# Optimization experiments

Hardware: AMD Instinct MI355X
Metric: run time of the kernel (lower is better)

Reference implementation:

```python
import jax, jax.numpy as jnp
import numpy as np

ROPE_BASE = 10000.0

def rotary_pe_3d(x, coords):
    # x: [B, H, L, D]; coords: [B, L, 3]. Split D into 3 axis chunks; rotate
    # each chunk (half-split pairs) by angles coord_axis * inv_freq.
    D = x.shape[-1]
    da = D // 3            # dims per spatial axis
    p = da // 2            # rotary pairs per axis
    inv_freq = 1.0 / (ROPE_BASE ** (jnp.arange(p, dtype=x.dtype) / p))  # [p]
    chunks = []
    for a in range(3):
        xa = x[..., a * da:(a + 1) * da]                       # [B,H,L,da]
        theta = coords[..., a][:, None, :, None] * inv_freq    # [B,1,L,p]
        cos, sin = jnp.cos(theta), jnp.sin(theta)
        x1, x2 = xa[..., :p], xa[..., p:]
        chunks.append(jnp.concatenate([x1 * cos - x2 * sin,
                                       x1 * sin + x2 * cos], axis=-1))
    if 3 * da < D:  # leave any remainder un-rotated
        chunks.append(x[..., 3 * da:])
    return jnp.concatenate(chunks, axis=-1)


def setup_inputs() -> dict:
    key = jax.random.key(0)
    ks = jax.random.split(key, 16)
    B, Lq, Lk, D, H = 4, 1024, 4096, 768, 8
    s = 1.0 / np.sqrt(D)
    return {
        "query": jax.random.normal(ks[0], (B, Lq, D), jnp.float32),
        "key": jax.random.normal(ks[1], (B, Lk, D), jnp.float32),
        "value": jax.random.normal(ks[2], (B, Lk, D), jnp.float32),
        "coords_query": jax.random.normal(ks[3], (B, Lq, 3), jnp.float32),
        "coords_key": jax.random.normal(ks[4], (B, Lk, 3), jnp.float32),
        "Wq": jax.random.normal(ks[5], (D, D), jnp.float32) * s,
        "bq": jnp.zeros((D,), jnp.float32),
        "Wk": jax.random.normal(ks[6], (D, D), jnp.float32) * s,
        "bk": jnp.zeros((D,), jnp.float32),
        "Wv": jax.random.normal(ks[7], (D, D), jnp.float32) * s,
        "bv": jnp.zeros((D,), jnp.float32),
        "Wo": jax.random.normal(ks[8], (D, D), jnp.float32) * s,
        "bo": jnp.zeros((D,), jnp.float32),
    }


def reference(query, key, value, coords_query, coords_key,
              Wq, bq, Wk, bk, Wv, bv, Wo, bo):
    B, Lq, D = query.shape
    Lk = key.shape[1]
    H = 8
    hd = D // H
    # Projections (nn.Linear: x @ W.T + b)
    q = (query @ Wq.T + bq).reshape(B, Lq, H, hd).transpose(0, 2, 1, 3)  # [B,H,Lq,hd]
    k = (key @ Wk.T + bk).reshape(B, Lk, H, hd).transpose(0, 2, 1, 3)
    v = (value @ Wv.T + bv).reshape(B, Lk, H, hd).transpose(0, 2, 1, 3)
    q = rotary_pe_3d(q, coords_query)
    k = rotary_pe_3d(k, coords_key)
    scores = jnp.einsum("bhqd,bhkd->bhqk", q, k) / jnp.sqrt(jnp.asarray(hd, q.dtype))
    attn = jax.nn.softmax(scores, axis=-1)  # dropout is identity in eval
    out = jnp.einsum("bhqk,bhkd->bhqd", attn, v)
    out = out.transpose(0, 2, 1, 3).reshape(B, Lq, D)
    return out @ Wo.T + bo
```

## Files before the change

### kernel.cpp

```cpp
#include <hip/hip_runtime.h>
#include <math.h>

#define DM 768
#define NH 8
#define HD 96
#define BQ 4
#define LQ 1024
#define LK 4096
#define BH (BQ*NH)
#define KVS 4
#define KC (LK/KVS)
#define NT (KC/64)
#define QB 128
#define NW (DM*DM)

typedef unsigned short ushort;
typedef unsigned int uint;
typedef __attribute__((ext_vector_type(8))) short short8v;
typedef __attribute__((ext_vector_type(4))) float float4v;

#define QSCALE 0.14724444641f

static __device__ __forceinline__ ushort f2bf(float x) {
    union { float f; uint u; } c; c.f = x;
    uint u = c.u;
    u += ((u >> 16) & 1u) + 0x7fffu;
    return (ushort)(u >> 16);
}

static __device__ __forceinline__ float bf2f(ushort x) {
    union { uint u; float f; } c; c.u = (uint)x << 16;
    return c.f;
}

static __device__ __forceinline__ uint cvtpk(float lo, float hi) {
    uint d;
    asm("v_cvt_pk_bf16_f32 %0, %1, %2" : "=v"(d) : "v"(lo), "v"(hi));
    return d;
}

static __device__ __forceinline__ float exp2hw(float x) {
#if __has_builtin(__builtin_amdgcn_exp2f)
    return __builtin_amdgcn_exp2f(x);
#else
    return __expf(x * 0.6931471805599453f);
#endif
}

static __device__ __forceinline__ void gload_lds16(const ushort* g, ushort* l) {
    __builtin_amdgcn_global_load_lds(
        (const __attribute__((address_space(1))) uint*)g,
        (__attribute__((address_space(3))) uint*)l, 16, 0, 0);
}

__global__ __launch_bounds__(256)
void wcvt(const float* __restrict__ w0, const float* __restrict__ w1,
          const float* __restrict__ w2, const float* __restrict__ w3,
          ushort* __restrict__ d)
{
    const int SEG = NW / 1024;
    int b = blockIdx.x;
    int wsel = b / SEG, ib = b % SEG;
    const float* s = (wsel == 0) ? w0 : (wsel == 1) ? w1 : (wsel == 2) ? w2 : w3;
    int i = ib * 256 + threadIdx.x;
    float4 v = ((const float4*)s)[i];
    uint2 o;
    o.x = (uint)f2bf(v.x) | ((uint)f2bf(v.y) << 16);
    o.y = (uint)f2bf(v.z) | ((uint)f2bf(v.w) << 16);
    ((uint2*)(d + (size_t)wsel * NW))[i] = o;
}

__global__ __launch_bounds__(256, 2)
void qkv_gemm(const float* __restrict__ qf, const float* __restrict__ kf,
              const float* __restrict__ vf,
              const ushort* __restrict__ wqb, const ushort* __restrict__ wkb,
              const ushort* __restrict__ wvb,
              const float* __restrict__ bq, const float* __restrict__ bk,
              const float* __restrict__ bv,
              const float* __restrict__ cq, const float* __restrict__ ck,
              ushort* __restrict__ qws, ushort* __restrict__ kws,
              ushort* __restrict__ vtb)
{
    __shared__ ushort Sh[16384];
    ushort* As = Sh;
    ushort* Bs = Sh + 8192;

    const int tid  = threadIdx.x;
    const int w    = tid >> 6;
    const int lane = tid & 63;
    const int l15  = lane & 15;
    const int lg   = lane >> 4;
    const int wm   = w >> 1, wn = w & 1;

    const int L = blockIdx.x;
    int seg, idx, Lshift, rpx;
    const float* X32; const ushort* Wbp; const float* bias; const float* coords;
    ushort* out; float oscale;
    if (L < 192)      { seg = 0; idx = L;       X32 = qf; Wbp = wqb; bias = bq; coords = cq; out = qws; Lshift = 10; rpx = 4;  oscale = QSCALE; }
    else if (L < 960) { seg = 1; idx = L - 192; X32 = kf; Wbp = wkb; bias = bk; coords = ck; out = kws; Lshift = 12; rpx = 16; oscale = 1.0f; }
    else              { seg = 2; idx = L - 960; X32 = vf; Wbp = wvb; bias = bv; coords = 0;  out = vtb; Lshift = 12; rpx = 16; oscale = 1.0f; }

    const int xcd  = idx & 7;
    const int sq   = idx >> 3;
    const int col0 = (sq % 6) * 128;
    const int row0 = (xcd * rpx + sq / 6) * 128;

    float4v acc[4][4];
    #pragma unroll
    for (int m = 0; m < 4; ++m)
        #pragma unroll
        for (int n = 0; n < 4; ++n) acc[m][n] = (float4v)0.f;

    int Pp[4], rrS[4], cbS[4];
    #pragma unroll
    for (int c = 0; c < 4; ++c) {
        int P = ((w*4 + c) << 10) + lane*16;
        int lgc = P ^ (((P >> 9) & 3) << 5);
        Pp[c]  = P;
        rrS[c] = lgc >> 7;
        cbS[c] = (lgc & 127) >> 1;
    }
    const float*  xb = X32 + (size_t)row0 * DM;
    const ushort* wb = Wbp + (size_t)col0 * DM;

    int offA[2][4], offB[2][4];
    #pragma unroll
    for (int kk = 0; kk < 2; ++kk) {
        #pragma unroll
        for (int m = 0; m < 4; ++m) {
            int byte = (wm*64 + m*16 + l15)*128 + kk*64 + lg*16;
            offA[kk][m] = byte ^ (((byte >> 9) & 3) << 5);
            byte = (wn*64 + m*16 + l15)*128 + kk*64 + lg*16;
            offB[kk][m] = byte ^ (((byte >> 9) & 3) << 5);
        }
    }

    for (int kt = 0; kt < DM; kt += 64) {
        float4 fa[4], fb[4];
        #pragma unroll
        for (int c = 0; c < 4; ++c) {
            const float* src = xb + (size_t)rrS[c]*DM + kt + cbS[c];
            fa[c] = *(const float4*)src;
            fb[c] = *(const float4*)(src + 4);
        }
        #pragma unroll
        for (int c = 0; c < 4; ++c)
            gload_lds16(wb + (size_t)rrS[c]*DM + kt + cbS[c], (ushort*)((char*)Bs + Pp[c]));
        #pragma unroll
        for (int c = 0; c < 4; ++c) {
            uint4 pk;
            pk.x = cvtpk(fa[c].x, fa[c].y);
            pk.y = cvtpk(fa[c].z, fa[c].w);
            pk.z = cvtpk(fb[c].x, fb[c].y);
            pk.w = cvtpk(fb[c].z, fb[c].w);
            *(uint4*)((char*)As + Pp[c]) = pk;
        }
        __syncthreads();
        #pragma unroll
        for (int kk = 0; kk < 2; ++kk) {
            short8v af[4], bfm[4];
            #pragma unroll
            for (int m = 0; m < 4; ++m)
                af[m] = *(const short8v*)((const char*)As + offA[kk][m]);
            #pragma unroll
            for (int n = 0; n < 4; ++n)
                bfm[n] = *(const short8v*)((const char*)Bs + offB[kk][n]);
            #pragma unroll
            for (int m = 0; m < 4; ++m)
                #pragma unroll
                for (int n = 0; n < 4; ++n)
                    acc[m][n] = __builtin_amdgcn_mfma_f32_16x16x32_bf16(af[m], bfm[n], acc[m][n], 0, 0, 0);
        }
        __syncthreads();
    }

    const int colbase = col0 + wn*64;
    float bvv[4];
    #pragma unroll
    for (int nt = 0; nt < 4; ++nt) bvv[nt] = bias[colbase + nt*16 + l15];
    #pragma unroll
    for (int m = 0; m < 4; ++m)
        #pragma unroll
        for (int nt = 0; nt < 4; ++nt)
            #pragma unroll
            for (int r = 0; r < 4; ++r) acc[m][nt][r] += bvv[nt];

    if (seg < 2) {
        const float freq = exp2f(-(float)l15 * 0.83048202372184058696f);
        const int a0 = ((colbase >> 5) + 0) % 3;
        const int a1 = ((colbase >> 5) + 1) % 3;
        const int F  = (colbase >> 4) & 1;
        #pragma unroll
        for (int m = 0; m < 4; ++m) {
            #pragma unroll
            for (int r = 0; r < 4; ++r) {
                int row = row0 + wm*64 + m*16 + lg*4 + r;
                const float* c3 = coords + (size_t)row * 3;
                float sn0, cs0, sn1, cs1;
                __sincosf(c3[a0] * freq, &sn0, &cs0);
                __sincosf(c3[a1] * freq, &sn1, &cs1);
                {
                    float A_ = F ? acc[m][1][r] : acc[m][0][r];
                    float B_ = F ? acc[m][0][r] : acc[m][1][r];
                    float x1 = (A_*cs0 - B_*sn0) * oscale, x2 = (A_*sn0 + B_*cs0) * oscale;
                    if (F) { acc[m][1][r] = x1; acc[m][0][r] = x2; }
                    else   { acc[m][0][r] = x1; acc[m][1][r] = x2; }
                }
                {
                    float A_ = F ? acc[m][3][r] : acc[m][2][r];
                    float B_ = F ? acc[m][2][r] : acc[m][3][r];
                    float x1 = (A_*cs1 - B_*sn1) * oscale, x2 = (A_*sn1 + B_*cs1) * oscale;
                    if (F) { acc[m][3][r] = x1; acc[m][2][r] = x2; }
                    else   { acc[m][2][r] = x1; acc[m][3][r] = x2; }
                }
            }
        }
        const int Lm1 = (1 << Lshift) - 1;
        int hh[4], tt[4];
        #pragma unroll
        for (int nt = 0; nt < 4; ++nt) {
            int j0 = colbase + nt*16;
            hh[nt] = j0 / HD;
            tt[nt] = j0 % HD + l15;
        }
        #pragma unroll
        for (int m = 0; m < 4; ++m)
            #pragma unroll
            for (int r = 0; r < 4; ++r) {
                int row = row0 + wm*64 + m*16 + lg*4 + r;
                int b = row >> Lshift, l = row & Lm1;
                #pragma unroll
                for (int nt = 0; nt < 4; ++nt)
                    out[(((size_t)b*NH + hh[nt]) << Lshift | l) * HD + tt[nt]] =
                        f2bf(acc[m][nt][r]);
            }
    } else {
        #pragma unroll
        for (int m = 0; m < 4; ++m)
            #pragma unroll
            for (int nt = 0; nt < 4; ++nt)
                #pragma unroll
                for (int r = 0; r < 4; ++r) {
                    int c  = wn*64 + nt*16 + l15;
                    int ri = wm*64 + m*16 + lg*4 + r;
                    *(ushort*)((char*)Sh + c*256 + (((ri>>3) ^ (c&7))<<4) + (ri&7)*2)
                        = f2bf(acc[m][nt][r]);
                }
        __syncthreads();
        #pragma unroll
        for (int e = 0; e < 8; ++e) {
            int idx2 = tid + 256*e;
            int c = idx2 >> 4, r8 = idx2 & 15;
            uint4 val = *(const uint4*)((const char*)Sh + c*256 + ((r8 ^ (c&7))<<4));
            int j = col0 + c;
            int h = j / HD, t = j % HD;
            int row = row0 + r8*8;
            int b = row >> 12, l = row & (LK-1);
            *(uint4*)&out[(((size_t)b*NH + h)*HD + t)*LK + l] = val;
        }
    }
}

__global__ __launch_bounds__(256)
void gemm_out(const ushort* __restrict__ X, const ushort* __restrict__ Wb,
              const float* __restrict__ bias, float* __restrict__ out)
{
    __shared__ ushort Sh[16384];
    ushort* As = Sh;
    ushort* Bs = Sh + 8192;

    const int tid  = threadIdx.x;
    const int w    = tid >> 6;
    const int lane = tid & 63;
    const int l15  = lane & 15;
    const int lg   = lane >> 4;
    const int wm   = w >> 1, wn = w & 1;

    const int L    = blockIdx.x;
    const int xcd  = L & 7;
    const int sq   = L >> 3;
    const int col0 = (sq % 6) * 128;
    const int row0 = (xcd * 4 + sq / 6) * 128;

    float4v acc[4][4];
    #pragma unroll
    for (int m = 0; m < 4; ++m)
        #pragma unroll
        for (int n = 0; n < 4; ++n) acc[m][n] = (float4v)0.f;

    int Pp[4], rrS[4], cbS[4];
    #pragma unroll
    for (int c = 0; c < 4; ++c) {
        int P = ((w*4 + c) << 10) + lane*16;
        int lgc = P ^ (((P >> 9) & 3) << 5);
        Pp[c]  = P;
        rrS[c] = lgc >> 7;
        cbS[c] = (lgc & 127) >> 1;
    }
    const ushort* xb = X  + (size_t)row0 * DM;
    const ushort* wb = Wb + (size_t)col0 * DM;

    int offA[2][4], offB[2][4];
    #pragma unroll
    for (int kk = 0; kk < 2; ++kk) {
        #pragma unroll
        for (int m = 0; m < 4; ++m) {
            int byte = (wm*64 + m*16 + l15)*128 + kk*64 + lg*16;
            offA[kk][m] = byte ^ (((byte >> 9) & 3) << 5);
            byte = (wn*64 + m*16 + l15)*128 + kk*64 + lg*16;
            offB[kk][m] = byte ^ (((byte >> 9) & 3) << 5);
        }
    }

    for (int kt = 0; kt < DM; kt += 64) {
        #pragma unroll
        for (int c = 0; c < 4; ++c) {
            gload_lds16(xb + (size_t)rrS[c]*DM + kt + cbS[c], (ushort*)((char*)As + Pp[c]));
            gload_lds16(wb + (size_t)rrS[c]*DM + kt + cbS[c], (ushort*)((char*)Bs + Pp[c]));
        }
        __syncthreads();
        #pragma unroll
        for (int kk = 0; kk < 2; ++kk) {
            short8v af[4], bfm[4];
            #pragma unroll
            for (int m = 0; m < 4; ++m)
                af[m] = *(const short8v*)((const char*)As + offA[kk][m]);
            #pragma unroll
            for (int n = 0; n < 4; ++n)
                bfm[n] = *(const short8v*)((const char*)Bs + offB[kk][n]);
            #pragma unroll
            for (int m = 0; m < 4; ++m)
                #pragma unroll
                for (int n = 0; n < 4; ++n)
                    acc[m][n] = __builtin_amdgcn_mfma_f32_16x16x32_bf16(af[m], bfm[n], acc[m][n], 0, 0, 0);
        }
        __syncthreads();
    }

    const int colbase = col0 + wn*64;
    float bvv[4];
    #pragma unroll
    for (int nt = 0; nt < 4; ++nt) bvv[nt] = bias[colbase + nt*16 + l15];
    #pragma unroll
    for (int m = 0; m < 4; ++m)
        #pragma unroll
        for (int r = 0; r < 4; ++r) {
            int row = row0 + wm*64 + m*16 + lg*4 + r;
            #pragma unroll
            for (int nt = 0; nt < 4; ++nt)
                out[(size_t)row*DM + colbase + nt*16 + l15] = acc[m][nt][r] + bvv[nt];
        }
}

__global__ __launch_bounds__(256, 2)
void attn_mfma(const ushort* __restrict__ q, const ushort* __restrict__ k,
               const ushort* __restrict__ vt, ushort* __restrict__ opb,
               float* __restrict__ mlb)
{
    __shared__ ushort Ks[64*128];
    __shared__ ushort Vs[96*64];
    __shared__ ushort PsT[4][32][72];

    const int tid  = threadIdx.x;
    const int w    = tid >> 6;
    const int lane = tid & 63;
    const int l15  = lane & 15;
    const int lg   = lane >> 4;

    const int L   = blockIdx.x;
    const int xcd = L & 7;
    const int s   = L >> 3;
    const int pr  = xcd*16 + (s >> 3);
    const int qt  = s & 7;
    const int bh  = pr & 31;
    const int sc  = pr >> 5;

    const ushort* qg = q  + ((size_t)bh * LQ + qt*QB + w*32 + l15) * HD;
    const ushort* kg = k  + ((size_t)bh * LK + (size_t)sc * KC) * HD;
    const ushort* vg = vt + (size_t)bh * HD * LK + (size_t)sc * KC;

    short8v aq0[3], aq1[3];
    #pragma unroll
    for (int dc = 0; dc < 3; ++dc) {
        aq0[dc] = *(const short8v*)(qg + dc*32 + lg*8);
        aq1[dc] = *(const short8v*)(qg + 16*HD + dc*32 + lg*8);
    }

    int kdst[3], ksrc[3], vdst[3], vsrc[3];
    #pragma unroll
    for (int j = 0; j < 3; ++j) {
        int c = tid + 256*j;
        int kr = c / 12, ks = c % 12;
        kdst[j] = kr*256 + ((ks ^ (kr & 7)) << 4);
        ksrc[j] = kr*HD + ks*8;
        int vr = c >> 3, vs = c & 7;
        vdst[j] = vr*128 + ((vs ^ (vr & 7)) << 4);
        vsrc[j] = vr*LK + vs*8;
    }
    int tK[3], tV[2];
    #pragma unroll
    for (int dc = 0; dc < 3; ++dc) tK[dc] = ((dc*4 + lg) ^ (l15 & 7)) << 4;
    #pragma unroll
    for (int h2 = 0; h2 < 2; ++h2)  tV[h2] = ((h2*4 + lg) ^ (l15 & 7)) << 4;

    float4v o0[6], o1[6];
    #pragma unroll
    for (int dt = 0; dt < 6; ++dt) { o0[dt] = (float4v)0.f; o1[dt] = (float4v)0.f; }
    float m_0 = -1e30f, l_0 = 0.f;
    float m_1 = -1e30f, l_1 = 0.f;

    short8v kreg[3], vreg[3];
    #pragma unroll
    for (int j = 0; j < 3; ++j) {
        kreg[j] = *(const short8v*)(kg + ksrc[j]);
        vreg[j] = *(const short8v*)(vg + vsrc[j]);
    }
    #pragma unroll
    for (int j = 0; j < 3; ++j) {
        *(short8v*)((char*)Ks + kdst[j]) = kreg[j];
        *(short8v*)((char*)Vs + vdst[j]) = vreg[j];
    }
    __syncthreads();

    for (int t = 0; t < NT; ++t) {
        if (t + 1 < NT) {
            const ushort* kn = kg + (size_t)(t+1)*64*HD;
            const ushort* vn = vg + (t+1)*64;
            #pragma unroll
            for (int j = 0; j < 3; ++j) {
                kreg[j] = *(const short8v*)(kn + ksrc[j]);
                vreg[j] = *(const short8v*)(vn + vsrc[j]);
            }
        }

        float4v s0[4], s1[4];
        __builtin_amdgcn_s_setprio(1);
        #pragma unroll
        for (int nt = 0; nt < 4; ++nt) {
            s0[nt] = (float4v)0.f;
            s1[nt] = (float4v)0.f;
            #pragma unroll
            for (int dc = 0; dc < 3; ++dc) {
                short8v bk = *(const short8v*)((const char*)Ks + nt*4096 + l15*256 + tK[dc]);
                s0[nt] = __builtin_amdgcn_mfma_f32_16x16x32_bf16(bk, aq0[dc], s0[nt], 0, 0, 0);
                s1[nt] = __builtin_amdgcn_mfma_f32_16x16x32_bf16(bk, aq1[dc], s1[nt], 0, 0, 0);
            }
        }
        __builtin_amdgcn_s_setprio(0);

        float mt0 = -1e30f, mt1 = -1e30f;
        #pragma unroll
        for (int nt = 0; nt < 4; ++nt)
            #pragma unroll
            for (int r = 0; r < 4; ++r) {
                mt0 = fmaxf(mt0, s0[nt][r]);
                mt1 = fmaxf(mt1, s1[nt][r]);
            }
        mt0 = fmaxf(mt0, __shfl_xor(mt0, 16, 64));
        mt0 = fmaxf(mt0, __shfl_xor(mt0, 32, 64));
        mt1 = fmaxf(mt1, __shfl_xor(mt1, 16, 64));
        mt1 = fmaxf(mt1, __shfl_xor(mt1, 32, 64));

        if (__any((mt0 > m_0 + 11.5f) || (mt1 > m_1 + 11.5f))) {
            float mn0 = fmaxf(m_0, mt0), mn1 = fmaxf(m_1, mt1);
            float a0 = exp2hw(m_0 - mn0), a1 = exp2hw(m_1 - mn1);
            m_0 = mn0; m_1 = mn1;
            l_0 *= a0;  l_1 *= a1;
            float al0[4], al1[4];
            #pragma unroll
            for (int r = 0; r < 4; ++r) {
                al0[r] = __shfl(a0, lg*4 + r, 64);
                al1[r] = __shfl(a1, lg*4 + r, 64);
            }
            #pragma unroll
            for (int dt = 0; dt < 6; ++dt)
                #pragma unroll
                for (int r = 0; r < 4; ++r) {
                    o0[dt][r] *= al0[r];
                    o1[dt][r] *= al1[r];
                }
        }

        float ps0 = 0.f, ps1 = 0.f;
        #pragma unroll
        for (int nt = 0; nt < 4; ++nt)
            #pragma unroll
            for (int r = 0; r < 4; ++r) {
                float p0 = exp2hw(s0[nt][r] - m_0);
                float p1 = exp2hw(s1[nt][r] - m_1);
                s0[nt][r] = p0; ps0 += p0;
                s1[nt][r] = p1; ps1 += p1;
            }
        ps0 += __shfl_xor(ps0, 16, 64);
        ps0 += __shfl_xor(ps0, 32, 64);
        ps1 += __shfl_xor(ps1, 16, 64);
        ps1 += __shfl_xor(ps1, 32, 64);
        l_0 += ps0;
        l_1 += ps1;

        #pragma unroll
        for (int nt = 0; nt < 4; ++nt) {
            uint2 pk0, pk1;
            pk0.x = cvtpk(s0[nt][0], s0[nt][1]);
            pk0.y = cvtpk(s0[nt][2], s0[nt][3]);
            pk1.x = cvtpk(s1[nt][0], s1[nt][1]);
            pk1.y = cvtpk(s1[nt][2], s1[nt][3]);
            *(uint2*)&PsT[w][l15][nt*16 + lg*4]      = pk0;
            *(uint2*)&PsT[w][16 + l15][nt*16 + lg*4] = pk1;
        }

        short8v a00 = *(const short8v*)&PsT[w][l15][lg*8];
        short8v a01 = *(const short8v*)&PsT[w][l15][32 + lg*8];
        short8v a10 = *(const short8v*)&PsT[w][16 + l15][lg*8];
        short8v a11 = *(const short8v*)&PsT[w][16 + l15][32 + lg*8];
        __builtin_amdgcn_s_setprio(1);
        #pragma unroll
        for (int dt = 0; dt < 6; ++dt) {
            short8v bv0 = *(const short8v*)((const char*)Vs + dt*2048 + l15*128 + tV[0]);
            short8v bv1 = *(const short8v*)((const char*)Vs + dt*2048 + l15*128 + tV[1]);
            o0[dt] = __builtin_amdgcn_mfma_f32_16x16x32_bf16(a00, bv0, o0[dt], 0, 0, 0);
            o0[dt] = __builtin_amdgcn_mfma_f32_16x16x32_bf16(a01, bv1, o0[dt], 0, 0, 0);
            o1[dt] = __builtin_amdgcn_mfma_f32_16x16x32_bf16(a10, bv0, o1[dt], 0, 0, 0);
            o1[dt] = __builtin_amdgcn_mfma_f32_16x16x32_bf16(a11, bv1, o1[dt], 0, 0, 0);
        }
        __builtin_amdgcn_s_setprio(0);
        __syncthreads();

        if (t + 1 < NT) {
            #pragma unroll
            for (int j = 0; j < 3; ++j) {
                *(short8v*)((char*)Ks + kdst[j]) = kreg[j];
                *(short8v*)((char*)Vs + vdst[j]) = vreg[j];
            }
        }
        __syncthreads();
    }

    ushort* ob = opb + (((size_t)sc * BH + bh) * LQ + qt*QB + w*32) * HD;
    #pragma unroll
    for (int r = 0; r < 4; ++r) {
        #pragma unroll
        for (int dt = 0; dt < 6; ++dt) {
            ob[(size_t)(lg*4 + r) * HD + dt*16 + l15]      = f2bf(o0[dt][r]);
            ob[(size_t)(16 + lg*4 + r) * HD + dt*16 + l15] = f2bf(o1[dt][r]);
        }
    }
    if (lane < 16) {
        size_t mlrow = ((size_t)sc * BH + bh) * LQ + qt*QB + w*32 + lane;
        mlb[mlrow*2 + 0] = m_0;
        mlb[mlrow*2 + 1] = l_0;
        mlb[(mlrow + 16)*2 + 0] = m_1;
        mlb[(mlrow + 16)*2 + 1] = l_1;
    }
}

__global__ __launch_bounds__(256)
void combine(const ushort* __restrict__ opb, const float* __restrict__ mlb,
             ushort* __restrict__ ctx)
{
    const int NROW = BH * LQ;
    int idx = blockIdx.x * 256 + threadIdx.x;
    int row = idx / 12, seg = idx % 12;

    float m[KVS], lv[KVS];
    #pragma unroll
    for (int i = 0; i < KVS; ++i) {
        m[i]  = mlb[((size_t)i*NROW + row)*2 + 0];
        lv[i] = mlb[((size_t)i*NROW + row)*2 + 1];
    }
    float ms = m[0];
    #pragma unroll
    for (int i = 1; i < KVS; ++i) ms = fmaxf(ms, m[i]);
    float wsum = 0.f, wgt[KVS];
    #pragma unroll
    for (int i = 0; i < KVS; ++i) {
        wgt[i] = exp2hw(m[i] - ms);
        wsum += lv[i] * wgt[i];
    }
    float inv = 1.f / wsum;

    float acc[8] = {};
    #pragma unroll
    for (int i = 0; i < KVS; ++i) {
        uint4 v = *(const uint4*)&opb[((size_t)i*NROW + row)*HD + seg*8];
        uint vv[4] = {v.x, v.y, v.z, v.w};
        #pragma unroll
        for (int j2 = 0; j2 < 4; ++j2) {
            acc[j2*2+0] += bf2f((ushort)(vv[j2] & 0xffff)) * wgt[i];
            acc[j2*2+1] += bf2f((ushort)(vv[j2] >> 16))    * wgt[i];
        }
    }

    int bh = row / LQ, l = row % LQ;
    int b = bh >> 3, h = bh & 7;
    ushort* o = ctx + ((size_t)b * LQ + l) * DM + h * HD + seg*8;
    uint4 pk;
    pk.x = cvtpk(acc[0]*inv, acc[1]*inv);
    pk.y = cvtpk(acc[2]*inv, acc[3]*inv);
    pk.z = cvtpk(acc[4]*inv, acc[5]*inv);
    pk.w = cvtpk(acc[6]*inv, acc[7]*inv);
    *(uint4*)o = pk;
}

extern "C" void kernel_launch(void* const* d_in, const int* in_sizes, int n_in,
                              void* d_out, int out_size, void* d_ws, size_t ws_size,
                              hipStream_t stream)
{
    const float* query = (const float*)d_in[0];
    const float* key   = (const float*)d_in[1];
    const float* value = (const float*)d_in[2];
    const float* cq    = (const float*)d_in[3];
    const float* ck    = (const float*)d_in[4];
    const float* Wq    = (const float*)d_in[5];
    const float* bqv   = (const float*)d_in[6];
    const float* Wk    = (const float*)d_in[7];
    const float* bkv   = (const float*)d_in[8];
    const float* Wv    = (const float*)d_in[9];
    const float* bvv   = (const float*)d_in[10];
    const float* Wo    = (const float*)d_in[11];
    const float* bov   = (const float*)d_in[12];
    float* out = (float*)d_out;

    const size_t NQ = (size_t)BQ * LQ * DM;
    const size_t NK = (size_t)BQ * LK * DM;
    const size_t NP = (size_t)KVS * BH * LQ * HD;

    ushort* wq  = (ushort*)d_ws;
    ushort* wk  = wq  + NW;
    ushort* wv  = wk  + NW;
    ushort* wo  = wv  + NW;
    ushort* qws = wo  + NW;
    ushort* kws = qws + NQ;
    ushort* vtb = kws + NK;
    ushort* opb = vtb + NK;
    ushort* ctx = opb + NP;
    float*  mlb = (float*)(ctx + NQ);

    wcvt<<<4*(NW/1024), 256, 0, stream>>>(Wq, Wk, Wv, Wo, wq);
    qkv_gemm<<<1728, 256, 0, stream>>>(query, key, value, wq, wk, wv,
                                       bqv, bkv, bvv, cq, ck, qws, kws, vtb);
    attn_mfma<<<(LQ/QB) * BH * KVS, 256, 0, stream>>>(qws, kws, vtb, opb, mlb);
    combine<<<BH*LQ*12/256, 256, 0, stream>>>(opb, mlb, ctx);
    gemm_out<<<(BQ*LQ/128)*6, 256, 0, stream>>>(ctx, wo, bov, out);
}
```

Before: 171.1 us.

## Software-pipeline QKV GEMM K-loop with double-buffered weight tiles in LDS

Restructures the qkv_gemm K loop so the next weight tile is loaded asynchronously into a second LDS buffer and the next fp32 activation tile is fetched into registers while MFMAs run on the current tile. The activation tile is converted to bf16 and stored after a barrier, which adds one extra __syncthreads per step. It also raises launch_bounds occupancy from 2 to 3 blocks per CU, which may add register pressure and spills, given the live prefetch registers and the 48KB of shared memory.

```diff
diff --git a/kernel.cpp b/kernel.cpp
--- a/kernel.cpp
+++ b/kernel.cpp
@@ -13,6 +13,7 @@
 #define NT (KC/64)
 #define QB 128
 #define NW (DM*DM)
+#define NKSTEP (DM/64)
 
 typedef unsigned short ushort;
 typedef unsigned int uint;
@@ -70,7 +71,7 @@
     ((uint2*)(d + (size_t)wsel * NW))[i] = o;
 }
 
-__global__ __launch_bounds__(256, 2)
+__global__ __launch_bounds__(256, 3)
 void qkv_gemm(const float* __restrict__ qf, const float* __restrict__ kf,
               const float* __restrict__ vf,
               const ushort* __restrict__ wqb, const ushort* __restrict__ wkb,
@@ -81,9 +82,7 @@
               ushort* __restrict__ qws, ushort* __restrict__ kws,
               ushort* __restrict__ vtb)
 {
-    __shared__ ushort Sh[16384];
-    ushort* As = Sh;
-    ushort* Bs = Sh + 8192;
+    __shared__ ushort Sh[24576];
 
     const int tid  = threadIdx.x;
     const int w    = tid >> 6;
@@ -135,36 +134,51 @@
         }
     }
 
-    for (int kt = 0; kt < DM; kt += 64) {
-        float4 fa[4], fb[4];
-        #pragma unroll
-        for (int c = 0; c < 4; ++c) {
-            const float* src = xb + (size_t)rrS[c]*DM + kt + cbS[c];
-            fa[c] = *(const float4*)src;
-            fb[c] = *(const float4*)(src + 4);
-        }
-        #pragma unroll
-        for (int c = 0; c < 4; ++c)
-            gload_lds16(wb + (size_t)rrS[c]*DM + kt + cbS[c], (ushort*)((char*)Bs + Pp[c]));
-        #pragma unroll
-        for (int c = 0; c < 4; ++c) {
-            uint4 pk;
-            pk.x = cvtpk(fa[c].x, fa[c].y);
-            pk.y = cvtpk(fa[c].z, fa[c].w);
-            pk.z = cvtpk(fb[c].x, fb[c].y);
-            pk.w = cvtpk(fb[c].z, fb[c].w);
-            *(uint4*)((char*)As + Pp[c]) = pk;
-        }
-        __syncthreads();
+    float4 fa[4], fb[4];
+    #pragma unroll
+    for (int c = 0; c < 4; ++c) {
+        const float* src = xb + (size_t)rrS[c]*DM + cbS[c];
+        fa[c] = *(const float4*)src;
+        fb[c] = *(const float4*)(src + 4);
+    }
+    #pragma unroll
+    for (int c = 0; c < 4; ++c)
+        gload_lds16(wb + (size_t)rrS[c]*DM + cbS[c], (ushort*)((char*)Sh + 16384 + Pp[c]));
+    #pragma unroll
+    for (int c = 0; c < 4; ++c) {
+        uint4 pk;
+        pk.x = cvtpk(fa[c].x, fa[c].y);
+        pk.y = cvtpk(fa[c].z, fa[c].w);
+        pk.z = cvtpk(fb[c].x, fb[c].y);
+        pk.w = cvtpk(fb[c].z, fb[c].w);
+        *(uint4*)((char*)Sh + Pp[c]) = pk;
+    }
+    __syncthreads();
+
+    for (int t = 0; t < NKSTEP; ++t) {
+        const int bbase = 16384 + ((t & 1) << 14);
+        if (t + 1 < NKSTEP) {
+            const int nb = 16384 + (((t + 1) & 1) << 14);
+            #pragma unroll
+            for (int c = 0; c < 4; ++c)
+                gload_lds16(wb + (size_t)rrS[c]*DM + (t+1)*64 + cbS[c],
+                            (ushort*)((char*)Sh + nb + Pp[c]));
+            #pragma unroll
+            for (int c = 0; c < 4; ++c) {
+                const float* src = xb + (size_t)rrS[c]*DM + (t+1)*64 + cbS[c];
+                fa[c] = *(const float4*)src;
+                fb[c] = *(const float4*)(src + 4);
+            }
+        }
         #pragma unroll
         for (int kk = 0; kk < 2; ++kk) {
             short8v af[4], bfm[4];
             #pragma unroll
             for (int m = 0; m < 4; ++m)
-                af[m] = *(const short8v*)((const char*)As + offA[kk][m]);
+                af[m] = *(const short8v*)((const char*)Sh + offA[kk][m]);
             #pragma unroll
             for (int n = 0; n < 4; ++n)
-                bfm[n] = *(const short8v*)((const char*)Bs + offB[kk][n]);
+                bfm[n] = *(const short8v*)((const char*)Sh + bbase + offB[kk][n]);
             #pragma unroll
             for (int m = 0; m < 4; ++m)
                 #pragma unroll
@@ -172,6 +186,18 @@
                     acc[m][n] = __builtin_amdgcn_mfma_f32_16x16x32_bf16(af[m], bfm[n], acc[m][n], 0, 0, 0);
         }
         __syncthreads();
+        if (t + 1 < NKSTEP) {
+            #pragma unroll
+            for (int c = 0; c < 4; ++c) {
+                uint4 pk;
+                pk.x = cvtpk(fa[c].x, fa[c].y);
+                pk.y = cvtpk(fa[c].z, fa[c].w);
+                pk.z = cvtpk(fb[c].x, fb[c].y);
+                pk.w = cvtpk(fb[c].z, fb[c].w);
+                *(uint4*)((char*)Sh + Pp[c]) = pk;
+            }
+            __syncthreads();
+        }
     }
 
     const int colbase = col0 + wn*64;
```

After: 174.9 us. +2.2%, slower.

## Load fp32 activations directly to LDS and convert to bf16 at fragment read

Applied to the files above, without the earlier changes.

The QKV projection GEMM now streams the fp32 activation tile straight into shared memory with global_load_lds, using a new XOR swizzle, instead of loading through registers and converting before the LDS store. The bf16 conversion moves to the MFMA fragment read, so each k-step does two fp32 LDS reads per fragment. The goal is to cut VGPR pressure and register staging so occupancy can rise to 3 blocks per CU. The cost is LDS growing to 48KB per block, doubled LDS read traffic for A, and conversions repeated in the inner loop.

```diff
diff --git a/kernel.cpp b/kernel.cpp
--- a/kernel.cpp
+++ b/kernel.cpp
@@ -13,6 +13,7 @@
 #define NT (KC/64)
 #define QB 128
 #define NW (DM*DM)
+#define NKSTEP (DM/64)
 
 typedef unsigned short ushort;
 typedef unsigned int uint;
@@ -47,7 +48,7 @@
 #endif
 }
 
-static __device__ __forceinline__ void gload_lds16(const ushort* g, ushort* l) {
+static __device__ __forceinline__ void gload_lds16(const void* g, void* l) {
     __builtin_amdgcn_global_load_lds(
         (const __attribute__((address_space(1))) uint*)g,
         (__attribute__((address_space(3))) uint*)l, 16, 0, 0);
@@ -70,7 +71,7 @@
     ((uint2*)(d + (size_t)wsel * NW))[i] = o;
 }
 
-__global__ __launch_bounds__(256, 2)
+__global__ __launch_bounds__(256, 3)
 void qkv_gemm(const float* __restrict__ qf, const float* __restrict__ kf,
               const float* __restrict__ vf,
               const ushort* __restrict__ wqb, const ushort* __restrict__ wkb,
@@ -81,9 +82,9 @@
               ushort* __restrict__ qws, ushort* __restrict__ kws,
               ushort* __restrict__ vtb)
 {
-    __shared__ ushort Sh[16384];
-    ushort* As = Sh;
-    ushort* Bs = Sh + 8192;
+    __shared__ ushort Sh[24576];
+    char* As = (char*)Sh;
+    char* Bs = (char*)Sh + 32768;
 
     const int tid  = threadIdx.x;
     const int w    = tid >> 6;
@@ -111,60 +112,67 @@
         #pragma unroll
         for (int n = 0; n < 4; ++n) acc[m][n] = (float4v)0.f;
 
-    int Pp[4], rrS[4], cbS[4];
+    int PA[8], rA[8], cA[8];
+    #pragma unroll
+    for (int c = 0; c < 8; ++c) {
+        int P = ((w*8 + c) << 10) + lane*16;
+        int r = P >> 8;
+        int j = ((P >> 4) & 15) ^ (r & 15);
+        PA[c] = P;
+        rA[c] = r;
+        cA[c] = j * 4;
+    }
+    int PB[4], rB[4], cB[4];
     #pragma unroll
     for (int c = 0; c < 4; ++c) {
         int P = ((w*4 + c) << 10) + lane*16;
         int lgc = P ^ (((P >> 9) & 3) << 5);
-        Pp[c]  = P;
-        rrS[c] = lgc >> 7;
-        cbS[c] = (lgc & 127) >> 1;
+        PB[c] = P;
+        rB[c] = lgc >> 7;
+        cB[c] = (lgc & 127) >> 1;
     }
     const float*  xb = X32 + (size_t)row0 * DM;
     const ushort* wb = Wbp + (size_t)col0 * DM;
 
-    int offA[2][4], offB[2][4];
+    int offA0[2][4], offA1[2][4], offB[2][4];
     #pragma unroll
     for (int kk = 0; kk < 2; ++kk) {
         #pragma unroll
         for (int m = 0; m < 4; ++m) {
-            int byte = (wm*64 + m*16 + l15)*128 + kk*64 + lg*16;
-            offA[kk][m] = byte ^ (((byte >> 9) & 3) << 5);
-            byte = (wn*64 + m*16 + l15)*128 + kk*64 + lg*16;
+            int R  = wm*64 + m*16 + l15;
+            int j0 = kk*8 + lg*2;
+            offA0[kk][m] = R*256 + (((j0    ) ^ (R & 15)) << 4);
+            offA1[kk][m] = R*256 + (((j0 + 1) ^ (R & 15)) << 4);
+            int byte = (wn*64 + m*16 + l15)*128 + kk*64 + lg*16;
             offB[kk][m] = byte ^ (((byte >> 9) & 3) << 5);
         }
     }
 
     for (int kt = 0; kt < DM; kt += 64) {
-        float4 fa[4], fb[4];
-        #pragma unroll
-        for (int c = 0; c < 4; ++c) {
-            const float* src = xb + (size_t)rrS[c]*DM + kt + cbS[c];
-            fa[c] = *(const float4*)src;
-            fb[c] = *(const float4*)(src + 4);
-        }
+        #pragma unroll
+        for (int c = 0; c < 8; ++c)
+            gload_lds16(xb + (size_t)rA[c]*DM + kt + cA[c], As + PA[c]);
         #pragma unroll
         for (int c = 0; c < 4; ++c)
-            gload_lds16(wb + (size_t)rrS[c]*DM + kt + cbS[c], (ushort*)((char*)Bs + Pp[c]));
-        #pragma unroll
-        for (int c = 0; c < 4; ++c) {
-            uint4 pk;
-            pk.x = cvtpk(fa[c].x, fa[c].y);
-            pk.y = cvtpk(fa[c].z, fa[c].w);
-            pk.z = cvtpk(fb[c].x, fb[c].y);
-            pk.w = cvtpk(fb[c].z, fb[c].w);
-            *(uint4*)((char*)As + Pp[c]) = pk;
-        }
+            gload_lds16(wb + (size_t)rB[c]*DM + kt + cB[c], Bs + PB[c]);
         __syncthreads();
         #pragma unroll
         for (int kk = 0; kk < 2; ++kk) {
             short8v af[4], bfm[4];
             #pragma unroll
-            for (int m = 0; m < 4; ++m)
-                af[m] = *(const short8v*)((const char*)As + offA[kk][m]);
+            for (int m = 0; m < 4; ++m) {
+                float4 x0 = *(const float4*)(As + offA0[kk][m]);
+                float4 x1 = *(const float4*)(As + offA1[kk][m]);
+                union { uint4 u; short8v s; } cv;
+                cv.u.x = cvtpk(x0.x, x0.y);
+                cv.u.y = cvtpk(x0.z, x0.w);
+                cv.u.z = cvtpk(x1.x, x1.y);
+                cv.u.w = cvtpk(x1.z, x1.w);
+                af[m] = cv.s;
+            }
             #pragma unroll
             for (int n = 0; n < 4; ++n)
-                bfm[n] = *(const short8v*)((const char*)Bs + offB[kk][n]);
+                bfm[n] = *(const short8v*)(Bs + offB[kk][n]);
             #pragma unroll
             for (int m = 0; m < 4; ++m)
                 #pragma unroll
@@ -243,7 +251,7 @@
                 for (int r = 0; r < 4; ++r) {
                     int c  = wn*64 + nt*16 + l15;
                     int ri = wm*64 + m*16 + lg*4 + r;
-                    *(ushort*)((char*)Sh + c*256 + (((ri>>3) ^ (c&7))<<4) + (ri&7)*2)
+                    *(ushort*)(As + c*256 + (((ri>>3) ^ (c&7))<<4) + (ri&7)*2)
                         = f2bf(acc[m][nt][r]);
                 }
         __syncthreads();
@@ -251,7 +259,7 @@
         for (int e = 0; e < 8; ++e) {
             int idx2 = tid + 256*e;
             int c = idx2 >> 4, r8 = idx2 & 15;
-            uint4 val = *(const uint4*)((const char*)Sh + c*256 + ((r8 ^ (c&7))<<4));
+            uint4 val = *(const uint4*)(As + c*256 + ((r8 ^ (c&7))<<4));
             int j = col0 + c;
             int h = j / HD, t = j % HD;
             int row = row0 + r8*8;
@@ -315,8 +323,8 @@
     for (int kt = 0; kt < DM; kt += 64) {
         #pragma unroll
         for (int c = 0; c < 4; ++c) {
-            gload_lds16(xb + (size_t)rrS[c]*DM + kt + cbS[c], (ushort*)((char*)As + Pp[c]));
-            gload_lds16(wb + (size_t)rrS[c]*DM + kt + cbS[c], (ushort*)((char*)Bs + Pp[c]));
+            gload_lds16(xb + (size_t)rrS[c]*DM + kt + cbS[c], (char*)As + Pp[c]);
+            gload_lds16(wb + (size_t)rrS[c]*DM + kt + cbS[c], (char*)Bs + Pp[c]);
         }
         __syncthreads();
         #pragma unroll
```

Measured after the change: 172.7 us. No clear change (+1.0%).

## Widen QKV projection GEMM tile to 128x256 to halve fp32 activation reloads

Applied to the files above, without the earlier changes.

The fused QKV projection kernel now computes 128x256 output tiles instead of 128x128, so each block converts its fp32 activation rows once for twice as many output columns. This halves the block count and the redundant global reads and bf16 conversion of the large fp32 inputs. In exchange each wave holds twice the accumulators, which raises register pressure under launch_bounds(256,2). The rotary and V-transpose epilogues are reworked to match, and the V transpose is staged through LDS in two column halves.

```diff
diff --git a/kernel.cpp b/kernel.cpp
--- a/kernel.cpp
+++ b/kernel.cpp
@@ -13,6 +13,7 @@
 #define NT (KC/64)
 #define QB 128
 #define NW (DM*DM)
+#define NKSTEP (DM/64)
 
 typedef unsigned short ushort;
 typedef unsigned int uint;
@@ -47,7 +48,7 @@
 #endif
 }
 
-static __device__ __forceinline__ void gload_lds16(const ushort* g, ushort* l) {
+static __device__ __forceinline__ void gload_lds16(const void* g, void* l) {
     __builtin_amdgcn_global_load_lds(
         (const __attribute__((address_space(1))) uint*)g,
         (__attribute__((address_space(3))) uint*)l, 16, 0, 0);
@@ -81,9 +82,9 @@
               ushort* __restrict__ qws, ushort* __restrict__ kws,
               ushort* __restrict__ vtb)
 {
-    __shared__ ushort Sh[16384];
-    ushort* As = Sh;
-    ushort* Bs = Sh + 8192;
+    __shared__ ushort Sh[24576];
+    char* As = (char*)Sh;
+    char* Bs = (char*)Sh + 16384;
 
     const int tid  = threadIdx.x;
     const int w    = tid >> 6;
@@ -96,14 +97,200 @@
     int seg, idx, Lshift, rpx;
     const float* X32; const ushort* Wbp; const float* bias; const float* coords;
     ushort* out; float oscale;
-    if (L < 192)      { seg = 0; idx = L;       X32 = qf; Wbp = wqb; bias = bq; coords = cq; out = qws; Lshift = 10; rpx = 4;  oscale = QSCALE; }
-    else if (L < 960) { seg = 1; idx = L - 192; X32 = kf; Wbp = wkb; bias = bk; coords = ck; out = kws; Lshift = 12; rpx = 16; oscale = 1.0f; }
-    else              { seg = 2; idx = L - 960; X32 = vf; Wbp = wvb; bias = bv; coords = 0;  out = vtb; Lshift = 12; rpx = 16; oscale = 1.0f; }
+    if (L < 96)       { seg = 0; idx = L;       X32 = qf; Wbp = wqb; bias = bq; coords = cq; out = qws; Lshift = 10; rpx = 4;  oscale = QSCALE; }
+    else if (L < 480) { seg = 1; idx = L - 96;  X32 = kf; Wbp = wkb; bias = bk; coords = ck; out = kws; Lshift = 12; rpx = 16; oscale = 1.0f; }
+    else              { seg = 2; idx = L - 480; X32 = vf; Wbp = wvb; bias = bv; coords = 0;  out = vtb; Lshift = 12; rpx = 16; oscale = 1.0f; }
 
     const int xcd  = idx & 7;
     const int sq   = idx >> 3;
+    const int col0 = (sq % 3) * 256;
+    const int row0 = (xcd * rpx + sq / 3) * 128;
+
+    float4v acc[4][8];
+    #pragma unroll
+    for (int m = 0; m < 4; ++m)
+        #pragma unroll
+        for (int n = 0; n < 8; ++n) acc[m][n] = (float4v)0.f;
+
+    int PA[4], rA[4], cA[4];
+    #pragma unroll
+    for (int c = 0; c < 4; ++c) {
+        int P = ((w*4 + c) << 10) + lane*16;
+        int lgc = P ^ (((P >> 9) & 3) << 5);
+        PA[c] = P;
+        rA[c] = lgc >> 7;
+        cA[c] = (lgc & 127) >> 1;
+    }
+    int PB[8], rB[8], cB[8];
+    #pragma unroll
+    for (int c = 0; c < 8; ++c) {
+        int P = ((w*8 + c) << 10) + lane*16;
+        int lgc = P ^ (((P >> 9) & 3) << 5);
+        PB[c] = P;
+        rB[c] = lgc >> 7;
+        cB[c] = (lgc & 127) >> 1;
+    }
+    const float*  xb = X32 + (size_t)row0 * DM;
+    const ushort* wb = Wbp + (size_t)col0 * DM;
+
+    int offA[2][4], offB[2][8];
+    #pragma unroll
+    for (int kk = 0; kk < 2; ++kk) {
+        #pragma unroll
+        for (int m = 0; m < 4; ++m) {
+            int byte = (wm*64 + m*16 + l15)*128 + kk*64 + lg*16;
+            offA[kk][m] = byte ^ (((byte >> 9) & 3) << 5);
+        }
+        #pragma unroll
+        for (int n = 0; n < 8; ++n) {
+            int byte = (wn*128 + n*16 + l15)*128 + kk*64 + lg*16;
+            offB[kk][n] = byte ^ (((byte >> 9) & 3) << 5);
+        }
+    }
+
+    for (int kt = 0; kt < DM; kt += 64) {
+        #pragma unroll
+        for (int c = 0; c < 8; ++c)
+            gload_lds16(wb + (size_t)rB[c]*DM + kt + cB[c], Bs + PB[c]);
+        float4 fa[4], fb[4];
+        #pragma unroll
+        for (int c = 0; c < 4; ++c) {
+            const float* src = xb + (size_t)rA[c]*DM + kt + cA[c];
+            fa[c] = *(const float4*)src;
+            fb[c] = *(const float4*)(src + 4);
+        }
+        #pragma unroll
+        for (int c = 0; c < 4; ++c) {
+            uint4 pk;
+            pk.x = cvtpk(fa[c].x, fa[c].y);
+            pk.y = cvtpk(fa[c].z, fa[c].w);
+            pk.z = cvtpk(fb[c].x, fb[c].y);
+            pk.w = cvtpk(fb[c].z, fb[c].w);
+            *(uint4*)(As + PA[c]) = pk;
+        }
+        __syncthreads();
+        #pragma unroll
+        for (int kk = 0; kk < 2; ++kk) {
+            short8v af[4], bfm[8];
+            #pragma unroll
+            for (int m = 0; m < 4; ++m)
+                af[m] = *(const short8v*)(As + offA[kk][m]);
+            #pragma unroll
+            for (int n = 0; n < 8; ++n)
+                bfm[n] = *(const short8v*)(Bs + offB[kk][n]);
+            #pragma unroll
+            for (int m = 0; m < 4; ++m)
+                #pragma unroll
+                for (int n = 0; n < 8; ++n)
+                    acc[m][n] = __builtin_amdgcn_mfma_f32_16x16x32_bf16(af[m], bfm[n], acc[m][n], 0, 0, 0);
+        }
+        __syncthreads();
+    }
+
+    const int colbase = col0 + wn*128;
+    float bvv[8];
+    #pragma unroll
+    for (int nt = 0; nt < 8; ++nt) bvv[nt] = bias[colbase + nt*16 + l15];
+    #pragma unroll
+    for (int m = 0; m < 4; ++m)
+        #pragma unroll
+        for (int nt = 0; nt < 8; ++nt)
+            #pragma unroll
+            for (int r = 0; r < 4; ++r) acc[m][nt][r] += bvv[nt];
+
+    if (seg < 2) {
+        const float freq = exp2f(-(float)l15 * 0.83048202372184058696f);
+        int ap[4];
+        #pragma unroll
+        for (int p = 0; p < 4; ++p) ap[p] = ((colbase >> 5) + p) % 3;
+        #pragma unroll
+        for (int m = 0; m < 4; ++m) {
+            #pragma unroll
+            for (int r = 0; r < 4; ++r) {
+                int row = row0 + wm*64 + m*16 + lg*4 + r;
+                const float* c3 = coords + (size_t)row * 3;
+                #pragma unroll
+                for (int p = 0; p < 4; ++p) {
+                    float sn, cs;
+                    __sincosf(c3[ap[p]] * freq, &sn, &cs);
+                    float A_ = acc[m][2*p][r], B_ = acc[m][2*p+1][r];
+                    acc[m][2*p][r]   = (A_*cs - B_*sn) * oscale;
+                    acc[m][2*p+1][r] = (A_*sn + B_*cs) * oscale;
+                }
+            }
+        }
+        const int Lm1 = (1 << Lshift) - 1;
+        int hh[8], tt[8];
+        #pragma unroll
+        for (int nt = 0; nt < 8; ++nt) {
+            int j0 = colbase + nt*16;
+            hh[nt] = j0 / HD;
+            tt[nt] = j0 % HD + l15;
+        }
+        #pragma unroll
+        for (int m = 0; m < 4; ++m)
+            #pragma unroll
+            for (int r = 0; r < 4; ++r) {
+                int row = row0 + wm*64 + m*16 + lg*4 + r;
+                int b = row >> Lshift, l = row & Lm1;
+                #pragma unroll
+                for (int nt = 0; nt < 8; ++nt)
+                    out[(((size_t)b*NH + hh[nt]) << Lshift | l) * HD + tt[nt]] =
+                        f2bf(acc[m][nt][r]);
+            }
+    } else {
+        #pragma unroll
+        for (int h2 = 0; h2 < 2; ++h2) {
+            __syncthreads();
+            if (wn == h2) {
+                #pragma unroll
+                for (int m = 0; m < 4; ++m)
+                    #pragma unroll
+                    for (int nt = 0; nt < 8; ++nt)
+                        #pragma unroll
+                        for (int r = 0; r < 4; ++r) {
+                            int c  = nt*16 + l15;
+                            int ri = wm*64 + m*16 + lg*4 + r;
+                            *(ushort*)((char*)Sh + c*256 + (((ri>>3) ^ (c&7))<<4) + (ri&7)*2)
+                                = f2bf(acc[m][nt][r]);
+                        }
+            }
+            __syncthreads();
+            #pragma unroll
+            for (int e = 0; e < 8; ++e) {
+                int idx2 = tid + 256*e;
+                int c = idx2 >> 4, r8 = idx2 & 15;
+                uint4 val = *(const uint4*)((const char*)Sh + c*256 + ((r8 ^ (c&7))<<4));
+                int j = col0 + h2*128 + c;
+                int h = j / HD, t = j % HD;
+                int row = row0 + r8*8;
+                int b = row >> 12, l = row & (LK-1);
+                *(uint4*)&out[(((size_t)b*NH + h)*HD + t)*LK + l] = val;
+            }
+        }
+    }
+}
+
+__global__ __launch_bounds__(256)
+void gemm_out(const ushort* __restrict__ X, const ushort* __restrict__ Wb,
+              const float* __restrict__ bias, float* __restrict__ out)
+{
+    __shared__ ushort Sh[16384];
+    char* As = (char*)Sh;
+    char* Bs = (char*)Sh + 16384;
+
+    const int tid  = threadIdx.x;
+    const int w    = tid >> 6;
+    const int lane = tid & 63;
+    const int l15  = lane & 15;
+    const int lg   = lane >> 4;
+    const int wm   = w >> 1, wn = w & 1;
+
+    const int L    = blockIdx.x;
+    const int xcd  = L & 7;
+    const int sq   = L >> 3;
     const int col0 = (sq % 6) * 128;
-    const int row0 = (xcd * rpx + sq / 6) * 128;
+    const int row0 = (xcd * 4 + sq / 6) * 128;
 
     float4v acc[4][4];
     #pragma unroll
@@ -120,8 +307,8 @@
         rrS[c] = lgc >> 7;
         cbS[c] = (lgc & 127) >> 1;
     }
-    const float*  xb = X32 + (size_t)row0 * DM;
-    const ushort* wb = Wbp + (size_t)col0 * DM;
+    const ushort* xb = X  + (size_t)row0 * DM;
+    const ushort* wb = Wb + (size_t)col0 * DM;
 
     int offA[2][4], offB[2][4];
     #pragma unroll
@@ -136,24 +323,10 @@
     }
 
     for (int kt = 0; kt < DM; kt += 64) {
-        float4 fa[4], fb[4];
         #pragma unroll
         for (int c = 0; c < 4; ++c) {
-            const float* src = xb + (size_t)rrS[c]*DM + kt + cbS[c];
-            fa[c] = *(const float4*)src;
-            fb[c] = *(const float4*)(src + 4);
-        }
-        #pragma unroll
-        for (int c = 0; c < 4; ++c)
-            gload_lds16(wb + (size_t)rrS[c]*DM + kt + cbS[c], (ushort*)((char*)Bs + Pp[c]));
-        #pragma unroll
-        for (int c = 0; c < 4; ++c) {
-            uint4 pk;
-            pk.x = cvtpk(fa[c].x, fa[c].y);
-            pk.y = cvtpk(fa[c].z, fa[c].w);
-            pk.z = cvtpk(fb[c].x, fb[c].y);
-            pk.w = cvtpk(fb[c].z, fb[c].w);
-            *(uint4*)((char*)As + Pp[c]) = pk;
+            gload_lds16(xb + (size_t)rrS[c]*DM + kt + cbS[c], As + Pp[c]);
+            gload_lds16(wb + (size_t)rrS[c]*DM + kt + cbS[c], Bs + Pp[c]);
         }
         __syncthreads();
         #pragma unroll
@@ -161,173 +334,10 @@
             short8v af[4], bfm[4];
             #pragma unroll
             for (int m = 0; m < 4; ++m)
-                af[m] = *(const short8v*)((const char*)As + offA[kk][m]);
+                af[m] = *(const short8v*)(As + offA[kk][m]);
             #pragma unroll
             for (int n = 0; n < 4; ++n)
-                bfm[n] = *(const short8v*)((const char*)Bs + offB[kk][n]);
-            #pragma unroll
-            for (int m = 0; m < 4; ++m)
-                #pragma unroll
-                for (int n = 0; n < 4; ++n)
-                    acc[m][n] = __builtin_amdgcn_mfma_f32_16x16x32_bf16(af[m], bfm[n], acc[m][n], 0, 0, 0);
-        }
-        __syncthreads();
-    }
-
-    const int colbase = col0 + wn*64;
-    float bvv[4];
-    #pragma unroll
-    for (int nt = 0; nt < 4; ++nt) bvv[nt] = bias[colbase + nt*16 + l15];
-    #pragma unroll
-    for (int m = 0; m < 4; ++m)
-        #pragma unroll
-        for (int nt = 0; nt < 4; ++nt)
-            #pragma unroll
-            for (int r = 0; r < 4; ++r) acc[m][nt][r] += bvv[nt];
-
-    if (seg < 2) {
-        const float freq = exp2f(-(float)l15 * 0.83048202372184058696f);
-        const int a0 = ((colbase >> 5) + 0) % 3;
-        const int a1 = ((colbase >> 5) + 1) % 3;
-        const int F  = (colbase >> 4) & 1;
-        #pragma unroll
-        for (int m = 0; m < 4; ++m) {
-            #pragma unroll
-            for (int r = 0; r < 4; ++r) {
-                int row = row0 + wm*64 + m*16 + lg*4 + r;
-                const float* c3 = coords + (size_t)row * 3;
-                float sn0, cs0, sn1, cs1;
-                __sincosf(c3[a0] * freq, &sn0, &cs0);
-                __sincosf(c3[a1] * freq, &sn1, &cs1);
-                {
-                    float A_ = F ? acc[m][1][r] : acc[m][0][r];
-                    float B_ = F ? acc[m][0][r] : acc[m][1][r];
-                    float x1 = (A_*cs0 - B_*sn0) * oscale, x2 = (A_*sn0 + B_*cs0) * oscale;
-                    if (F) { acc[m][1][r] = x1; acc[m][0][r] = x2; }
-                    else   { acc[m][0][r] = x1; acc[m][1][r] = x2; }
-                }
-                {
-                    float A_ = F ? acc[m][3][r] : acc[m][2][r];
-                    float B_ = F ? acc[m][2][r] : acc[m][3][r];
-                    float x1 = (A_*cs1 - B_*sn1) * oscale, x2 = (A_*sn1 + B_*cs1) * oscale;
-                    if (F) { acc[m][3][r] = x1; acc[m][2][r] = x2; }
-                    else   { acc[m][2][r] = x1; acc[m][3][r] = x2; }
-                }
-            }
-        }
-        const int Lm1 = (1 << Lshift) - 1;
-        int hh[4], tt[4];
-        #pragma unroll
-        for (int nt = 0; nt < 4; ++nt) {
-            int j0 = colbase + nt*16;
-            hh[nt] = j0 / HD;
-            tt[nt] = j0 % HD + l15;
-        }
-        #pragma unroll
-        for (int m = 0; m < 4; ++m)
-            #pragma unroll
-            for (int r = 0; r < 4; ++r) {
-                int row = row0 + wm*64 + m*16 + lg*4 + r;
-                int b = row >> Lshift, l = row & Lm1;
-                #pragma unroll
-                for (int nt = 0; nt < 4; ++nt)
-                    out[(((size_t)b*NH + hh[nt]) << Lshift | l) * HD + tt[nt]] =
-                        f2bf(acc[m][nt][r]);
-            }
-    } else {
-        #pragma unroll
-        for (int m = 0; m < 4; ++m)
-            #pragma unroll
-            for (int nt = 0; nt < 4; ++nt)
-                #pragma unroll
-                for (int r = 0; r < 4; ++r) {
-                    int c  = wn*64 + nt*16 + l15;
-                    int ri = wm*64 + m*16 + lg*4 + r;
-                    *(ushort*)((char*)Sh + c*256 + (((ri>>3) ^ (c&7))<<4) + (ri&7)*2)
-                        = f2bf(acc[m][nt][r]);
-                }
-        __syncthreads();
-        #pragma unroll
-        for (int e = 0; e < 8; ++e) {
-            int idx2 = tid + 256*e;
-            int c = idx2 >> 4, r8 = idx2 & 15;
-            uint4 val = *(const uint4*)((const char*)Sh + c*256 + ((r8 ^ (c&7))<<4));
-            int j = col0 + c;
-            int h = j / HD, t = j % HD;
-            int row = row0 + r8*8;
-            int b = row >> 12, l = row & (LK-1);
-            *(uint4*)&out[(((size_t)b*NH + h)*HD + t)*LK + l] = val;
-        }
-    }
-}
-
-__global__ __launch_bounds__(256)
-void gemm_out(const ushort* __restrict__ X, const ushort* __restrict__ Wb,
-              const float* __restrict__ bias, float* __restrict__ out)
-{
-    __shared__ ushort Sh[16384];
-    ushort* As = Sh;
-    ushort* Bs = Sh + 8192;
-
-    const int tid  = threadIdx.x;
-    const int w    = tid >> 6;
-    const int lane = tid & 63;
-    const int l15  = lane & 15;
-    const int lg   = lane >> 4;
-    const int wm   = w >> 1, wn = w & 1;
-
-    const int L    = blockIdx.x;
-    const int xcd  = L & 7;
-    const int sq   = L >> 3;
-    const int col0 = (sq % 6) * 128;
-    const int row0 = (xcd * 4 + sq / 6) * 128;
-
-    float4v acc[4][4];
-    #pragma unroll
-    for (int m = 0; m < 4; ++m)
-        #pragma unroll
-        for (int n = 0; n < 4; ++n) acc[m][n] = (float4v)0.f;
-
-    int Pp[4], rrS[4], cbS[4];
-    #pragma unroll
-    for (int c = 0; c < 4; ++c) {
-        int P = ((w*4 + c) << 10) + lane*16;
-        int lgc = P ^ (((P >> 9) & 3) << 5);
-        Pp[c]  = P;
-        rrS[c] = lgc >> 7;
-        cbS[c] = (lgc & 127) >> 1;
-    }
-    const ushort* xb = X  + (size_t)row0 * DM;
-    const ushort* wb = Wb + (size_t)col0 * DM;
-
-    int offA[2][4], offB[2][4];
-    #pragma unroll
-    for (int kk = 0; kk < 2; ++kk) {
-        #pragma unroll
-        for (int m = 0; m < 4; ++m) {
-            int byte = (wm*64 + m*16 + l15)*128 + kk*64 + lg*16;
-            offA[kk][m] = byte ^ (((byte >> 9) & 3) << 5);
-            byte = (wn*64 + m*16 + l15)*128 + kk*64 + lg*16;
-            offB[kk][m] = byte ^ (((byte >> 9) & 3) << 5);
-        }
-    }
-
-    for (int kt = 0; kt < DM; kt += 64) {
-        #pragma unroll
-        for (int c = 0; c < 4; ++c) {
-            gload_lds16(xb + (size_t)rrS[c]*DM + kt + cbS[c], (ushort*)((char*)As + Pp[c]));
-            gload_lds16(wb + (size_t)rrS[c]*DM + kt + cbS[c], (ushort*)((char*)Bs + Pp[c]));
-        }
-        __syncthreads();
-        #pragma unroll
-        for (int kk = 0; kk < 2; ++kk) {
-            short8v af[4], bfm[4];
-            #pragma unroll
-            for (int m = 0; m < 4; ++m)
-                af[m] = *(const short8v*)((const char*)As + offA[kk][m]);
-            #pragma unroll
-            for (int n = 0; n < 4; ++n)
-                bfm[n] = *(const short8v*)((const char*)Bs + offB[kk][n]);
+                bfm[n] = *(const short8v*)(Bs + offB[kk][n]);
             #pragma unroll
             for (int m = 0; m < 4; ++m)
                 #pragma unroll
@@ -637,8 +647,8 @@
     float*  mlb = (float*)(ctx + NQ);
 
     wcvt<<<4*(NW/1024), 256, 0, stream>>>(Wq, Wk, Wv, Wo, wq);
-    qkv_gemm<<<1728, 256, 0, stream>>>(query, key, value, wq, wk, wv,
-                                       bqv, bkv, bvv, cq, ck, qws, kws, vtb);
+    qkv_gemm<<<864, 256, 0, stream>>>(query, key, value, wq, wk, wv,
+                                      bqv, bkv, bvv, cq, ck, qws, kws, vtb);
     attn_mfma<<<(LQ/QB) * BH * KVS, 256, 0, stream>>>(qws, kws, vtb, opb, mlb);
     combine<<<BH*LQ*12/256, 256, 0, stream>>>(opb, mlb, ctx);
     gemm_out<<<(BQ*LQ/128)*6, 256, 0, stream>>>(ctx, wo, bov, out);
```

Measured after the change: 170.9 us. No clear change (-0.1%).
